# Performance work log

Hardware: AMD Instinct MI355X
Metric: run time of the kernel (lower is better)

## Reference

```python
import jax, jax.numpy as jnp
import numpy as np

N = 100000
E = 1600000
IN_F, HID, OUT_F = 256, 128, 64


def setup_inputs() -> dict:
    key = jax.random.key(0)
    k_x, k_e, k_w1, k_w2, k_b1, k_b2 = jax.random.split(key, 6)
    x = jax.random.normal(k_x, (N, IN_F), dtype=jnp.float32)
    edge_index = jax.random.randint(k_e, (2, E), 0, N, dtype=jnp.int32)
    # GCNConv params: lin has no bias in PyG; separate additive bias per layer.
    W1 = jax.random.normal(k_w1, (IN_F, HID), dtype=jnp.float32) / np.sqrt(IN_F)
    b1 = jax.random.normal(k_b1, (HID,), dtype=jnp.float32) * 0.01
    W2 = jax.random.normal(k_w2, (HID, OUT_F), dtype=jnp.float32) / np.sqrt(HID)
    b2 = jax.random.normal(k_b2, (OUT_F,), dtype=jnp.float32) * 0.01
    return {"x": x, "edge_index": edge_index, "W1": W1, "b1": b1, "W2": W2, "b2": b2}


def _gcn_norm(edge_index, num_nodes):
    # add self loops (improved=False -> weight 1.0), symmetric normalization
    loop = jnp.arange(num_nodes, dtype=edge_index.dtype)
    src = jnp.concatenate([edge_index[0], loop])
    dst = jnp.concatenate([edge_index[1], loop])
    w = jnp.ones(src.shape[0], dtype=jnp.float32)
    deg = jax.ops.segment_sum(w, dst, num_segments=num_nodes)
    dinv = jnp.where(deg > 0, jax.lax.rsqrt(deg), 0.0)
    norm = dinv[src] * w * dinv[dst]
    return src, dst, norm


def _gcn_layer(h, W, b, src, dst, norm, num_nodes):
    h = h @ W                               # [N, out]
    msg = h[src] * norm[:, None]            # [E+N, out] gather + scale
    out = jax.ops.segment_sum(msg, dst, num_segments=num_nodes)  # scatter-add
    return out + b


def reference(x, edge_index, W1, b1, W2, b2):
    # dropout is identity in eval mode
    src, dst, norm = _gcn_norm(edge_index, N)
    h = _gcn_layer(x, W1, b1, src, dst, norm, N)
    h = jax.nn.relu(h)
    out = _gcn_layer(h, W2, b2, src, dst, norm, N)
    return out
```

## Files before the change

### kernel.cpp

```cpp
#include <hip/hip_runtime.h>
#include <hip/hip_bf16.h>

#define N_NODES 100000
#define N_EDGES 1600000
#define IN_FEAT 256
#define HID_F   128
#define OUT_FT  64

#define NBUK   256
#define NPB    391
#define BUKCAP 8192
#define EPB    4096
#define G_BIN  ((N_EDGES + EPB - 1) / EPB)
#define G_GEMM ((N_NODES + 127) / 128)
#define G_CAST ((IN_FEAT * HID_F + HID_F * OUT_FT + 255) / 256)

typedef unsigned short u16;
typedef __attribute__((ext_vector_type(8))) unsigned short u16x8;
typedef __attribute__((ext_vector_type(8))) short short8;
typedef __attribute__((ext_vector_type(4))) float f32x4;

static __device__ inline u16 f2bf(float f) {
    __hip_bfloat16 h = __float2bfloat16(f);
    return *reinterpret_cast<u16*>(&h);
}
static __device__ inline float bf2f(u16 u) {
    union { unsigned u; float f; } c;
    c.u = ((unsigned)u) << 16;
    return c.f;
}


__global__ __launch_bounds__(256) void k_bin(const int* __restrict__ srcA,
                                             const int* __restrict__ dstA,
                                             int* __restrict__ gcur, int2* __restrict__ pairs,
                                             const float* __restrict__ W1,
                                             const float* __restrict__ W2,
                                             u16* __restrict__ W1t, u16* __restrict__ W2t) {
    if (blockIdx.x >= G_BIN) {
        int idx = (blockIdx.x - G_BIN) * 256 + threadIdx.x;
        if (idx < IN_FEAT * HID_F) {
            int k = idx / HID_F, n = idx % HID_F;
            W1t[n * IN_FEAT + k] = f2bf(W1[idx]);
        } else {
            int e2 = idx - IN_FEAT * HID_F;
            if (e2 < HID_F * OUT_FT) {
                int k = e2 / OUT_FT, n = e2 % OUT_FT;
                W2t[n * HID_F + k] = f2bf(W2[e2]);
            }
        }
        return;
    }
    __shared__ int lh[NBUK];
    int t = threadIdx.x;
    int e0 = blockIdx.x * EPB;
    if (t < NBUK) lh[t] = 0;
    __syncthreads();
#pragma unroll
    for (int i = 0; i < EPB / 256; i++) {
        int e = e0 + i * 256 + t;
        if (e < N_EDGES) atomicAdd(&lh[dstA[e] / NPB], 1);
    }
    __syncthreads();
    if (t < NBUK) {
        int c = lh[t];
        lh[t] = atomicAdd(&gcur[t], c);
    }
    __syncthreads();
#pragma unroll
    for (int i = 0; i < EPB / 256; i++) {
        int e = e0 + i * 256 + t;
        if (e < N_EDGES) {
            int d = dstA[e];
            int b = d / NPB;
            int p = atomicAdd(&lh[b], 1);
            if (p < BUKCAP) pairs[(size_t)b * BUKCAP + p] = make_int2(srcA[e], d);
        }
    }
}


__global__ __launch_bounds__(256) void k_bukscan(const int* __restrict__ gcur,
                                                 int* __restrict__ bbase) {
    __shared__ int sm[256];
    int t = threadIdx.x;
    int v = gcur[t];
    sm[t] = v;
    __syncthreads();
    for (int o = 1; o < 256; o <<= 1) {
        int u = (t >= o) ? sm[t - o] : 0;
        __syncthreads();
        sm[t] += u;
        __syncthreads();
    }
    bbase[t] = sm[t] - v;
    if (t == NBUK - 1) bbase[NBUK] = sm[t];
}


__global__ __launch_bounds__(256) void k_fillB(const int2* __restrict__ pairs,
                                               const int* __restrict__ gcnt,
                                               const int* __restrict__ bbase,
                                               int* __restrict__ offsets,
                                               float* __restrict__ dinv,
                                               int* __restrict__ csr) {
    __shared__ int hist[NPB];
    __shared__ int sm[256];
    int b = blockIdx.x, t = threadIdx.x;
    int nbase = b * NPB;
    int nn = min(NPB, N_NODES - nbase);
    int cnt = gcnt[b];
    int ebase = bbase[b];
    const int2* pb = pairs + (size_t)b * BUKCAP;

    for (int i = t; i < NPB; i += 256) hist[i] = 0;
    __syncthreads();
    for (int i = t; i < cnt; i += 256) atomicAdd(&hist[pb[i].y - nbase], 1);
    __syncthreads();

    int base2 = t * 2;
    int c0 = (base2 < NPB) ? hist[base2] : 0;
    int c1 = (base2 + 1 < NPB) ? hist[base2 + 1] : 0;
    int s = c0 + c1;
    sm[t] = s;
    __syncthreads();
    for (int o = 1; o < 256; o <<= 1) {
        int u = (t >= o) ? sm[t - o] : 0;
        __syncthreads();
        sm[t] += u;
        __syncthreads();
    }
    int run = ebase + sm[t] - s;
    __syncthreads();
    int cc[2] = {c0, c1};
#pragma unroll
    for (int q = 0; q < 2; q++) {
        int n = base2 + q;
        if (n < nn) {
            int g = nbase + n;
            offsets[g] = run;
            dinv[g] = rsqrtf((float)(cc[q] + 1));
            hist[n] = run;
            run += cc[q];
        }
    }
    __syncthreads();
    for (int i = t; i < cnt; i += 256) {
        int2 e = pb[i];
        int p = atomicAdd(&hist[e.y - nbase], 1);
        csr[p] = e.x;
    }
    if (b == NBUK - 1 && t == 0) offsets[N_NODES] = N_EDGES;
}


__global__ __launch_bounds__(256) void k_gemm1(const float* __restrict__ A,
                                               const u16* __restrict__ Bt,
                                               const float* __restrict__ dinv,
                                               u16* __restrict__ C) {
    __shared__ u16 As[128][40];
    __shared__ u16 Bs[128][40];
    int tid = threadIdx.x;
    int wv = tid >> 6, lane = tid & 63;
    int m16 = lane & 15, quad = lane >> 4;
    int row0 = blockIdx.x * 128;
    int r = tid >> 1, h = tid & 1;
    int grow_s = row0 + r;
    bool rok = grow_s < N_NODES;

    f32x4 acc[2][8];
#pragma unroll
    for (int i = 0; i < 2; i++)
#pragma unroll
        for (int j = 0; j < 8; j++) acc[i][j] = (f32x4)(0.f);

    for (int k0 = 0; k0 < IN_FEAT; k0 += 32) {
        f32x4 v0 = (f32x4)(0.f), v1 = v0, v2 = v0, v3 = v0;
        if (rok) {
            const f32x4* src = (const f32x4*)&A[(size_t)grow_s * IN_FEAT + k0 + h * 16];
            v0 = src[0]; v1 = src[1]; v2 = src[2]; v3 = src[3];
        }
        u16x8 p0, p1;
#pragma unroll
        for (int j = 0; j < 4; j++) {
            p0[j] = f2bf(v0[j]); p0[4 + j] = f2bf(v1[j]);
            p1[j] = f2bf(v2[j]); p1[4 + j] = f2bf(v3[j]);
        }
        *(u16x8*)&As[r][h * 16] = p0;
        *(u16x8*)&As[r][h * 16 + 8] = p1;
        const u16x8* bsrc = (const u16x8*)&Bt[(size_t)r * IN_FEAT + k0 + h * 16];
        *(u16x8*)&Bs[r][h * 16] = bsrc[0];
        *(u16x8*)&Bs[r][h * 16 + 8] = bsrc[1];
        __syncthreads();

        short8 af0 = *(const short8*)&As[32 * wv + m16][quad * 8];
        short8 af1 = *(const short8*)&As[32 * wv + 16 + m16][quad * 8];
#pragma unroll
        for (int ct = 0; ct < 8; ct++) {
            short8 bf = *(const short8*)&Bs[16 * ct + m16][quad * 8];
            acc[0][ct] = __builtin_amdgcn_mfma_f32_16x16x32_bf16(af0, bf, acc[0][ct], 0, 0, 0);
            acc[1][ct] = __builtin_amdgcn_mfma_f32_16x16x32_bf16(af1, bf, acc[1][ct], 0, 0, 0);
        }
        __syncthreads();
    }
#pragma unroll
    for (int rt = 0; rt < 2; rt++)
#pragma unroll
        for (int r4 = 0; r4 < 4; r4++) {
            int grow = row0 + 32 * wv + 16 * rt + quad * 4 + r4;
            if (grow < N_NODES) {
                float dv = dinv[grow];
#pragma unroll
                for (int ct = 0; ct < 8; ct++)
                    C[(size_t)grow * HID_F + 16 * ct + m16] = f2bf(acc[rt][ct][r4] * dv);
            }
        }
}


__global__ __launch_bounds__(256) void k_gemm2(const u16* __restrict__ A,
                                               const u16* __restrict__ Bt,
                                               const float* __restrict__ dinv,
                                               u16* __restrict__ C) {
    __shared__ u16 As[128][40];
    __shared__ u16 Bs[64][40];
    int tid = threadIdx.x;
    int wv = tid >> 6, lane = tid & 63;
    int m16 = lane & 15, quad = lane >> 4;
    int row0 = blockIdx.x * 128;
    int r = tid >> 1, h = tid & 1;
    int grow_s = row0 + r;
    bool rok = grow_s < N_NODES;
    int nb = tid >> 2, q = tid & 3;

    f32x4 acc[2][4];
#pragma unroll
    for (int i = 0; i < 2; i++)
#pragma unroll
        for (int j = 0; j < 4; j++) acc[i][j] = (f32x4)(0.f);

    for (int k0 = 0; k0 < HID_F; k0 += 32) {
        u16x8 a0 = (u16x8)(0), a1v = (u16x8)(0);
        if (rok) {
            const u16x8* src = (const u16x8*)&A[(size_t)grow_s * HID_F + k0 + h * 16];
            a0 = src[0]; a1v = src[1];
        }
        *(u16x8*)&As[r][h * 16] = a0;
        *(u16x8*)&As[r][h * 16 + 8] = a1v;
        *(u16x8*)&Bs[nb][q * 8] = *(const u16x8*)&Bt[(size_t)nb * HID_F + k0 + q * 8];
        __syncthreads();

        short8 af0 = *(const short8*)&As[32 * wv + m16][quad * 8];
        short8 af1 = *(const short8*)&As[32 * wv + 16 + m16][quad * 8];
#pragma unroll
        for (int ct = 0; ct < 4; ct++) {
            short8 bf = *(const short8*)&Bs[16 * ct + m16][quad * 8];
            acc[0][ct] = __builtin_amdgcn_mfma_f32_16x16x32_bf16(af0, bf, acc[0][ct], 0, 0, 0);
            acc[1][ct] = __builtin_amdgcn_mfma_f32_16x16x32_bf16(af1, bf, acc[1][ct], 0, 0, 0);
        }
        __syncthreads();
    }
#pragma unroll
    for (int rt = 0; rt < 2; rt++)
#pragma unroll
        for (int r4 = 0; r4 < 4; r4++) {
            int grow = row0 + 32 * wv + 16 * rt + quad * 4 + r4;
            if (grow < N_NODES) {
                float dv = dinv[grow];
#pragma unroll
                for (int ct = 0; ct < 4; ct++)
                    C[(size_t)grow * OUT_FT + 16 * ct + m16] = f2bf(acc[rt][ct][r4] * dv);
            }
        }
}


__global__ __launch_bounds__(256) void k_agg1(const u16* __restrict__ hs,
                                              const int* __restrict__ offsets,
                                              const int* __restrict__ csr,
                                              const float* __restrict__ dinv,
                                              const float* __restrict__ b,
                                              u16* __restrict__ out) {
    int wave = threadIdx.x >> 6;
    int lane = threadIdx.x & 63;
    int node = blockIdx.x * 4 + wave;
    if (node >= N_NODES) return;
    int g = lane >> 4;
    int fl = lane & 15;
    const int fo = fl * 8;
    int beg = offsets[node], end = offsets[node + 1];

    float acc[8];
#pragma unroll
    for (int i = 0; i < 8; i++) acc[i] = 0.f;

    int j = beg;
    for (; j + 8 <= end; j += 8) {
        int s0 = csr[j + g];
        int s1 = csr[j + 4 + g];
        u16x8 r0 = *(const u16x8*)&hs[(size_t)s0 * HID_F + fo];
        u16x8 r1 = *(const u16x8*)&hs[(size_t)s1 * HID_F + fo];
#pragma unroll
        for (int i = 0; i < 8; i++) acc[i] += bf2f(r0[i]) + bf2f(r1[i]);
    }
    for (; j < end; j += 4) {
        int idx = j + g;
        if (idx < end) {
            int s = csr[idx];
            u16x8 r0 = *(const u16x8*)&hs[(size_t)s * HID_F + fo];
#pragma unroll
            for (int i = 0; i < 8; i++) acc[i] += bf2f(r0[i]);
        }
    }
#pragma unroll
    for (int i = 0; i < 8; i++) {
        acc[i] += __shfl_xor(acc[i], 16, 64);
        acc[i] += __shfl_xor(acc[i], 32, 64);
    }
    u16x8 sr = *(const u16x8*)&hs[(size_t)node * HID_F + fo];
#pragma unroll
    for (int i = 0; i < 8; i++) acc[i] += bf2f(sr[i]);

    if (g == 0) {
        float dv = dinv[node];
        f32x4 b0 = *(const f32x4*)&b[fo];
        f32x4 b1 = *(const f32x4*)&b[fo + 4];
        u16x8 o;
#pragma unroll
        for (int i = 0; i < 4; i++) {
            o[i] = f2bf(fmaxf(dv * acc[i] + b0[i], 0.f));
            o[4 + i] = f2bf(fmaxf(dv * acc[4 + i] + b1[i], 0.f));
        }
        *(u16x8*)&out[(size_t)node * HID_F + fo] = o;
    }
}


__global__ __launch_bounds__(256) void k_agg2(const u16* __restrict__ hs,
                                              const int* __restrict__ offsets,
                                              const int* __restrict__ csr,
                                              const float* __restrict__ dinv,
                                              const float* __restrict__ b,
                                              float* __restrict__ out) {
    int wave = threadIdx.x >> 6;
    int lane = threadIdx.x & 63;
    int node = blockIdx.x * 4 + wave;
    if (node >= N_NODES) return;
    int g = lane >> 3;
    int fl = lane & 7;
    const int fo = fl * 8;
    int beg = offsets[node], end = offsets[node + 1];

    float acc[8];
#pragma unroll
    for (int i = 0; i < 8; i++) acc[i] = 0.f;

    int j = beg;
    for (; j + 16 <= end; j += 16) {
        int s0 = csr[j + g];
        int s1 = csr[j + 8 + g];
        u16x8 r0 = *(const u16x8*)&hs[(size_t)s0 * OUT_FT + fo];
        u16x8 r1 = *(const u16x8*)&hs[(size_t)s1 * OUT_FT + fo];
#pragma unroll
        for (int i = 0; i < 8; i++) acc[i] += bf2f(r0[i]) + bf2f(r1[i]);
    }
    for (; j < end; j += 8) {
        int idx = j + g;
        if (idx < end) {
            int s = csr[idx];
            u16x8 r0 = *(const u16x8*)&hs[(size_t)s * OUT_FT + fo];
#pragma unroll
            for (int i = 0; i < 8; i++) acc[i] += bf2f(r0[i]);
        }
    }
#pragma unroll
    for (int i = 0; i < 8; i++) {
        acc[i] += __shfl_xor(acc[i], 8, 64);
        acc[i] += __shfl_xor(acc[i], 16, 64);
        acc[i] += __shfl_xor(acc[i], 32, 64);
    }
    u16x8 sr = *(const u16x8*)&hs[(size_t)node * OUT_FT + fo];
#pragma unroll
    for (int i = 0; i < 8; i++) acc[i] += bf2f(sr[i]);

    if (g == 0) {
        float dv = dinv[node];
        f32x4 b0 = *(const f32x4*)&b[fo];
        f32x4 b1 = *(const f32x4*)&b[fo + 4];
        f32x4 o0, o1;
#pragma unroll
        for (int i = 0; i < 4; i++) {
            o0[i] = dv * acc[i] + b0[i];
            o1[i] = dv * acc[4 + i] + b1[i];
        }
        *(f32x4*)&out[(size_t)node * OUT_FT + fo] = o0;
        *(f32x4*)&out[(size_t)node * OUT_FT + fo + 4] = o1;
    }
}


extern "C" void kernel_launch(void* const* d_in, const int* in_sizes, int n_in,
                              void* d_out, int out_size, void* d_ws, size_t ws_size,
                              hipStream_t stream) {
    const float* x  = (const float*)d_in[0];
    const int*   ei = (const int*)d_in[1];
    const float* W1 = (const float*)d_in[2];
    const float* b1 = (const float*)d_in[3];
    const float* W2 = (const float*)d_in[4];
    const float* b2 = (const float*)d_in[5];
    float* out = (float*)d_out;

    char* ws = (char*)d_ws;
    int*   offsets = (int*)(ws + 0);
    float* dinv    = (float*)(ws + 400512);
    int*   csr     = (int*)(ws + 800512);
    u16*   W1t     = (u16*)(ws + 7200512);
    u16*   W2t     = (u16*)(ws + 7266048);
    int*   gcur    = (int*)(ws + 7282432);
    int*   bbase   = (int*)(ws + 7283456);
    u16*   hs1     = (u16*)(ws + 7284608);
    u16*   a1      = (u16*)(ws + 32884608);
    int2*  pairs   = (int2*)(ws + 32884608);
    u16*   hs2     = hs1;

    const int* srcA = ei;
    const int* dstA = ei + N_EDGES;

    hipMemsetAsync(gcur, 0, NBUK * sizeof(int), stream);

    k_bin<<<G_BIN + G_CAST, 256, 0, stream>>>(srcA, dstA, gcur, pairs, W1, W2, W1t, W2t);
    k_bukscan<<<1, 256, 0, stream>>>(gcur, bbase);
    k_fillB<<<NBUK, 256, 0, stream>>>(pairs, gcur, bbase, offsets, dinv, csr);

    k_gemm1<<<G_GEMM, 256, 0, stream>>>(x, W1t, dinv, hs1);
    k_agg1<<<(N_NODES + 3) / 4, 256, 0, stream>>>(hs1, offsets, csr, dinv, b1, a1);
    k_gemm2<<<G_GEMM, 256, 0, stream>>>(a1, W2t, dinv, hs2);
    k_agg2<<<(N_NODES + 3) / 4, 256, 0, stream>>>(hs2, offsets, csr, dinv, b2, out);
}
```

Measured before the change: 356.4 us.

## Slice aggregation by feature columns and fold bucket scan into fillB

The aggregation kernels are restructured so each block handles one 16-feature column slice for a chunk of 32 nodes, with each lane gathering 4 bytes instead of 16. Consecutive blocks share the same node chunk across slices, which is meant to improve cache locality of the gathered rows within a slice and spread the gather across more blocks. The separate single-block bucket scan kernel is removed and each fillB block recomputes the prefix sum itself, saving one launch. The trade-off is redundant CSR index reads across the eight slices and narrower per-lane memory transactions.

```diff
diff --git a/kernel.cpp b/kernel.cpp
--- a/kernel.cpp
+++ b/kernel.cpp
@@ -15,6 +15,12 @@
 #define G_GEMM ((N_NODES + 127) / 128)
 #define G_CAST ((IN_FEAT * HID_F + HID_F * OUT_FT + 255) / 256)
 
+#define NPW 8
+#define NPBLK (4 * NPW)
+#define NCHUNK1 ((N_NODES + NPBLK - 1) / NPBLK)
+#define HALF_N 50000
+#define NCHUNK2 ((HALF_N + NPBLK - 1) / NPBLK)
+
 typedef unsigned short u16;
 typedef __attribute__((ext_vector_type(8))) unsigned short u16x8;
 typedef __attribute__((ext_vector_type(8))) short short8;
@@ -24,10 +30,11 @@
     __hip_bfloat16 h = __float2bfloat16(f);
     return *reinterpret_cast<u16*>(&h);
 }
-static __device__ inline float bf2f(u16 u) {
-    union { unsigned u; float f; } c;
-    c.u = ((unsigned)u) << 16;
-    return c.f;
+static __device__ inline float bf_lo(unsigned r) {
+    union { unsigned u; float f; } c; c.u = r << 16; return c.f;
+}
+static __device__ inline float bf_hi(unsigned r) {
+    union { unsigned u; float f; } c; c.u = r & 0xffff0000u; return c.f;
 }
 
 
@@ -80,27 +87,8 @@
 }
 
 
-__global__ __launch_bounds__(256) void k_bukscan(const int* __restrict__ gcur,
-                                                 int* __restrict__ bbase) {
-    __shared__ int sm[256];
-    int t = threadIdx.x;
-    int v = gcur[t];
-    sm[t] = v;
-    __syncthreads();
-    for (int o = 1; o < 256; o <<= 1) {
-        int u = (t >= o) ? sm[t - o] : 0;
-        __syncthreads();
-        sm[t] += u;
-        __syncthreads();
-    }
-    bbase[t] = sm[t] - v;
-    if (t == NBUK - 1) bbase[NBUK] = sm[t];
-}
-
-
 __global__ __launch_bounds__(256) void k_fillB(const int2* __restrict__ pairs,
                                                const int* __restrict__ gcnt,
-                                               const int* __restrict__ bbase,
                                                int* __restrict__ offsets,
                                                float* __restrict__ dinv,
                                                int* __restrict__ csr) {
@@ -110,8 +98,18 @@
     int nbase = b * NPB;
     int nn = min(NPB, N_NODES - nbase);
     int cnt = gcnt[b];
-    int ebase = bbase[b];
     const int2* pb = pairs + (size_t)b * BUKCAP;
+
+    sm[t] = gcnt[t];
+    __syncthreads();
+    for (int o = 1; o < 256; o <<= 1) {
+        int u = (t >= o) ? sm[t - o] : 0;
+        __syncthreads();
+        sm[t] += u;
+        __syncthreads();
+    }
+    int ebase = sm[b] - cnt;
+    __syncthreads();
 
     for (int i = t; i < NPB; i += 256) hist[i] = 0;
     __syncthreads();
@@ -281,57 +279,51 @@
                                               const float* __restrict__ dinv,
                                               const float* __restrict__ b,
                                               u16* __restrict__ out) {
-    int wave = threadIdx.x >> 6;
-    int lane = threadIdx.x & 63;
-    int node = blockIdx.x * 4 + wave;
-    if (node >= N_NODES) return;
-    int g = lane >> 4;
-    int fl = lane & 15;
-    const int fo = fl * 8;
-    int beg = offsets[node], end = offsets[node + 1];
-
-    float acc[8];
-#pragma unroll
-    for (int i = 0; i < 8; i++) acc[i] = 0.f;
-
-    int j = beg;
-    for (; j + 8 <= end; j += 8) {
-        int s0 = csr[j + g];
-        int s1 = csr[j + 4 + g];
-        u16x8 r0 = *(const u16x8*)&hs[(size_t)s0 * HID_F + fo];
-        u16x8 r1 = *(const u16x8*)&hs[(size_t)s1 * HID_F + fo];
-#pragma unroll
-        for (int i = 0; i < 8; i++) acc[i] += bf2f(r0[i]) + bf2f(r1[i]);
-    }
-    for (; j < end; j += 4) {
-        int idx = j + g;
-        if (idx < end) {
-            int s = csr[idx];
-            u16x8 r0 = *(const u16x8*)&hs[(size_t)s * HID_F + fo];
-#pragma unroll
-            for (int i = 0; i < 8; i++) acc[i] += bf2f(r0[i]);
-        }
-    }
-#pragma unroll
-    for (int i = 0; i < 8; i++) {
-        acc[i] += __shfl_xor(acc[i], 16, 64);
-        acc[i] += __shfl_xor(acc[i], 32, 64);
-    }
-    u16x8 sr = *(const u16x8*)&hs[(size_t)node * HID_F + fo];
-#pragma unroll
-    for (int i = 0; i < 8; i++) acc[i] += bf2f(sr[i]);
-
-    if (g == 0) {
-        float dv = dinv[node];
-        f32x4 b0 = *(const f32x4*)&b[fo];
-        f32x4 b1 = *(const f32x4*)&b[fo + 4];
-        u16x8 o;
-#pragma unroll
-        for (int i = 0; i < 4; i++) {
-            o[i] = f2bf(fmaxf(dv * acc[i] + b0[i], 0.f));
-            o[4 + i] = f2bf(fmaxf(dv * acc[4 + i] + b1[i], 0.f));
-        }
-        *(u16x8*)&out[(size_t)node * HID_F + fo] = o;
+    int slice = blockIdx.x & 7;
+    int chunk = blockIdx.x >> 3;
+    int wave = threadIdx.x >> 6, lane = threadIdx.x & 63;
+    int g = lane >> 3;
+    int fl = lane & 7;
+    int fbase = slice * 16 + fl * 2;
+    float bx = b[fbase], by = b[fbase + 1];
+    int node0 = chunk * NPBLK + wave * NPW;
+
+    for (int ni = 0; ni < NPW; ni++) {
+        int node = node0 + ni;
+        if (node >= N_NODES) return;
+        int beg = offsets[node], end = offsets[node + 1];
+        float ax = 0.f, ay = 0.f;
+        int j = beg;
+        for (; j + 16 <= end; j += 16) {
+            int s0 = csr[j + g], s1 = csr[j + 8 + g];
+            unsigned r0 = *(const unsigned*)&hs[(size_t)s0 * HID_F + fbase];
+            unsigned r1 = *(const unsigned*)&hs[(size_t)s1 * HID_F + fbase];
+            ax += bf_lo(r0) + bf_lo(r1);
+            ay += bf_hi(r0) + bf_hi(r1);
+        }
+        for (; j < end; j += 8) {
+            int idx = j + g;
+            if (idx < end) {
+                int s = csr[idx];
+                unsigned r0 = *(const unsigned*)&hs[(size_t)s * HID_F + fbase];
+                ax += bf_lo(r0);
+                ay += bf_hi(r0);
+            }
+        }
+#pragma unroll
+        for (int m = 8; m < 64; m <<= 1) {
+            ax += __shfl_xor(ax, m, 64);
+            ay += __shfl_xor(ay, m, 64);
+        }
+        unsigned sr = *(const unsigned*)&hs[(size_t)node * HID_F + fbase];
+        ax += bf_lo(sr);
+        ay += bf_hi(sr);
+        if (g == 0) {
+            float dv = dinv[node];
+            unsigned o = (unsigned)f2bf(fmaxf(dv * ax + bx, 0.f)) |
+                         ((unsigned)f2bf(fmaxf(dv * ay + by, 0.f)) << 16);
+            *(unsigned*)&out[(size_t)node * HID_F + fbase] = o;
+        }
     }
 }
 
@@ -342,59 +334,54 @@
                                               const float* __restrict__ dinv,
                                               const float* __restrict__ b,
                                               float* __restrict__ out) {
-    int wave = threadIdx.x >> 6;
-    int lane = threadIdx.x & 63;
-    int node = blockIdx.x * 4 + wave;
-    if (node >= N_NODES) return;
+    int col = blockIdx.x & 7;
+    int slice = col & 3;
+    int half = col >> 2;
+    int chunk = blockIdx.x >> 3;
+    int wave = threadIdx.x >> 6, lane = threadIdx.x & 63;
     int g = lane >> 3;
     int fl = lane & 7;
-    const int fo = fl * 8;
-    int beg = offsets[node], end = offsets[node + 1];
-
-    float acc[8];
-#pragma unroll
-    for (int i = 0; i < 8; i++) acc[i] = 0.f;
-
-    int j = beg;
-    for (; j + 16 <= end; j += 16) {
-        int s0 = csr[j + g];
-        int s1 = csr[j + 8 + g];
-        u16x8 r0 = *(const u16x8*)&hs[(size_t)s0 * OUT_FT + fo];
-        u16x8 r1 = *(const u16x8*)&hs[(size_t)s1 * OUT_FT + fo];
-#pragma unroll
-        for (int i = 0; i < 8; i++) acc[i] += bf2f(r0[i]) + bf2f(r1[i]);
-    }
-    for (; j < end; j += 8) {
-        int idx = j + g;
-        if (idx < end) {
-            int s = csr[idx];
-            u16x8 r0 = *(const u16x8*)&hs[(size_t)s * OUT_FT + fo];
-#pragma unroll
-            for (int i = 0; i < 8; i++) acc[i] += bf2f(r0[i]);
-        }
-    }
-#pragma unroll
-    for (int i = 0; i < 8; i++) {
-        acc[i] += __shfl_xor(acc[i], 8, 64);
-        acc[i] += __shfl_xor(acc[i], 16, 64);
-        acc[i] += __shfl_xor(acc[i], 32, 64);
-    }
-    u16x8 sr = *(const u16x8*)&hs[(size_t)node * OUT_FT + fo];
-#pragma unroll
-    for (int i = 0; i < 8; i++) acc[i] += bf2f(sr[i]);
-
-    if (g == 0) {
-        float dv = dinv[node];
-        f32x4 b0 = *(const f32x4*)&b[fo];
-        f32x4 b1 = *(const f32x4*)&b[fo + 4];
-        f32x4 o0, o1;
-#pragma unroll
-        for (int i = 0; i < 4; i++) {
-            o0[i] = dv * acc[i] + b0[i];
-            o1[i] = dv * acc[4 + i] + b1[i];
-        }
-        *(f32x4*)&out[(size_t)node * OUT_FT + fo] = o0;
-        *(f32x4*)&out[(size_t)node * OUT_FT + fo + 4] = o1;
+    int fbase = slice * 16 + fl * 2;
+    float bx = b[fbase], by = b[fbase + 1];
+    int node0 = half * HALF_N + chunk * NPBLK + wave * NPW;
+
+    for (int ni = 0; ni < NPW; ni++) {
+        int node = node0 + ni;
+        if (node >= N_NODES) return;
+        int beg = offsets[node], end = offsets[node + 1];
+        float ax = 0.f, ay = 0.f;
+        int j = beg;
+        for (; j + 16 <= end; j += 16) {
+            int s0 = csr[j + g], s1 = csr[j + 8 + g];
+            unsigned r0 = *(const unsigned*)&hs[(size_t)s0 * OUT_FT + fbase];
+            unsigned r1 = *(const unsigned*)&hs[(size_t)s1 * OUT_FT + fbase];
+            ax += bf_lo(r0) + bf_lo(r1);
+            ay += bf_hi(r0) + bf_hi(r1);
+        }
+        for (; j < end; j += 8) {
+            int idx = j + g;
+            if (idx < end) {
+                int s = csr[idx];
+                unsigned r0 = *(const unsigned*)&hs[(size_t)s * OUT_FT + fbase];
+                ax += bf_lo(r0);
+                ay += bf_hi(r0);
+            }
+        }
+#pragma unroll
+        for (int m = 8; m < 64; m <<= 1) {
+            ax += __shfl_xor(ax, m, 64);
+            ay += __shfl_xor(ay, m, 64);
+        }
+        unsigned sr = *(const unsigned*)&hs[(size_t)node * OUT_FT + fbase];
+        ax += bf_lo(sr);
+        ay += bf_hi(sr);
+        if (g == 0) {
+            float dv = dinv[node];
+            float2 o;
+            o.x = dv * ax + bx;
+            o.y = dv * ay + by;
+            *(float2*)&out[(size_t)node * OUT_FT + fbase] = o;
+        }
     }
 }
 
@@ -417,7 +404,6 @@
     u16*   W1t     = (u16*)(ws + 7200512);
     u16*   W2t     = (u16*)(ws + 7266048);
     int*   gcur    = (int*)(ws + 7282432);
-    int*   bbase   = (int*)(ws + 7283456);
     u16*   hs1     = (u16*)(ws + 7284608);
     u16*   a1      = (u16*)(ws + 32884608);
     int2*  pairs   = (int2*)(ws + 32884608);
@@ -429,11 +415,10 @@
     hipMemsetAsync(gcur, 0, NBUK * sizeof(int), stream);
 
     k_bin<<<G_BIN + G_CAST, 256, 0, stream>>>(srcA, dstA, gcur, pairs, W1, W2, W1t, W2t);
-    k_bukscan<<<1, 256, 0, stream>>>(gcur, bbase);
-    k_fillB<<<NBUK, 256, 0, stream>>>(pairs, gcur, bbase, offsets, dinv, csr);
+    k_fillB<<<NBUK, 256, 0, stream>>>(pairs, gcur, offsets, dinv, csr);
 
     k_gemm1<<<G_GEMM, 256, 0, stream>>>(x, W1t, dinv, hs1);
-    k_agg1<<<(N_NODES + 3) / 4, 256, 0, stream>>>(hs1, offsets, csr, dinv, b1, a1);
+    k_agg1<<<NCHUNK1 * 8, 256, 0, stream>>>(hs1, offsets, csr, dinv, b1, a1);
     k_gemm2<<<G_GEMM, 256, 0, stream>>>(a1, W2t, dinv, hs2);
-    k_agg2<<<(N_NODES + 3) / 4, 256, 0, stream>>>(hs2, offsets, csr, dinv, b2, out);
-}
+    k_agg2<<<NCHUNK2 * 8, 256, 0, stream>>>(hs2, offsets, csr, dinv, b2, out);
+}
```

New measurement: 629.9 us. 1.77x slower.
